# Optimization experiments

Hardware: AMD Instinct MI355X
Metric: run time of the kernel (lower is better)

Reference implementation:

```python
import jax, jax.numpy as jnp
import numpy as np

WIDTH = 256
FREQS = 10
INPUT_WIDTH = 3 + 3 * 2 * FREQS  # 63


def embed_point(point, freqs):
    # point: [N, 3] -> [N, 3*(1+2*freqs)]
    linear = point[..., None]                                  # [N, 3, 1]
    scales = jnp.exp2(jnp.arange(freqs, dtype=point.dtype))    # [freqs]
    angles = linear * scales                                   # [N, 3, freqs]
    emb = jnp.concatenate((linear, jnp.sin(angles), jnp.cos(angles)), axis=-1)
    return emb.reshape(*point.shape[:-1], 3 * (1 + 2 * freqs))


def _xavier(key, fan_in, fan_out):
    limit = jnp.sqrt(6.0 / (fan_in + fan_out)).astype(jnp.float32)
    return jax.random.uniform(key, (fan_in, fan_out), jnp.float32, -limit, limit)


def setup_inputs() -> dict:
    key = jax.random.key(0)
    keys = jax.random.split(key, 20)
    N = 524288
    point = jax.random.normal(keys[0], (N, 3), dtype=jnp.float32)
    dims = [
        (INPUT_WIDTH, WIDTH), (WIDTH, WIDTH), (WIDTH, WIDTH), (WIDTH, WIDTH),
        (WIDTH, WIDTH), (WIDTH + INPUT_WIDTH, WIDTH), (WIDTH, WIDTH),
        (WIDTH, WIDTH), (WIDTH, 4),
    ]
    inp = {"point": point}
    for i, (fi, fo) in enumerate(dims):
        inp[f"w{i}"] = _xavier(keys[1 + i], fi, fo)
        inp[f"b{i}"] = jnp.zeros((fo,), dtype=jnp.float32)
    return inp


def reference(point, w0, b0, w1, b1, w2, b2, w3, b3, w4, b4,
              w5, b5, w6, b6, w7, b7, w8, b8):
    inp = embed_point(point, FREQS)                 # [N, 63]
    x = jax.nn.relu(inp @ w0 + b0)
    x = jax.nn.relu(x @ w1 + b1)
    x = jax.nn.relu(x @ w2 + b2)
    x = jax.nn.relu(x @ w3 + b3)
    x = jax.nn.relu(x @ w4 + b4)
    x = jax.nn.relu(jnp.concatenate((x, inp), -1) @ w5 + b5)  # skip concat
    x = jax.nn.relu(x @ w6 + b6)
    x = jax.nn.relu(x @ w7 + b7)
    return x @ w8 + b8                              # [N, 4]
```

## Files before the change

kernel.cpp:

```cpp
#include <hip/hip_runtime.h>
#include <math.h>


typedef __attribute__((ext_vector_type(8))) short short8;
typedef __attribute__((ext_vector_type(4))) float f32x4;
typedef __attribute__((ext_vector_type(16))) float f32x16;

struct WPtrs { const float* w[8]; };
struct BPtrs { const float* b[8]; };

#define INV2PI 0.15915494309189533577f

#define PK_L0 0
#define PK_L1 16384
#define PK_L2 81920
#define PK_L3 147456
#define PK_L4 212992
#define PK_L5 278528
#define PK_L6 360448
#define PK_L7 425984
#define PK_W8 491520
#define PK_TOTAL 495616

__device__ __forceinline__ unsigned short f2bf(float v) {
  unsigned u = __float_as_uint(v);
  u = u + 0x7fffu + ((u >> 16) & 1u);
  return (unsigned short)(u >> 16);
}
__device__ __forceinline__ float bf_lo(unsigned u) { return __uint_as_float(u << 16); }
__device__ __forceinline__ float bf_hi(unsigned u) { return __uint_as_float(u & 0xffff0000u); }

__device__ __forceinline__ unsigned cvtpk(float a, float b) {
#if __has_builtin(__builtin_amdgcn_cvt_pk_bf16_f32)
  typedef __attribute__((ext_vector_type(2))) __bf16 bf16x2_t;
  bf16x2_t r = __builtin_amdgcn_cvt_pk_bf16_f32(a, b);
  return __builtin_bit_cast(unsigned, r);
#else
  unsigned ua = __float_as_uint(a);
  ua += 0x7fffu + ((ua >> 16) & 1u);
  unsigned ub = __float_as_uint(b);
  ub += 0x7fffu + ((ub >> 16) & 1u);
#if __has_builtin(__builtin_amdgcn_perm)
  return __builtin_amdgcn_perm(ub, ua, 0x07060302u);
#else
  return (ua >> 16) | (ub & 0xffff0000u);
#endif
#endif
}

__device__ __forceinline__ float fractf_(float x) {
#if __has_builtin(__builtin_amdgcn_fract_f32)
  return __builtin_amdgcn_fract_f32(x);
#else
  return x - floorf(x);
#endif
}
__device__ __forceinline__ float sin_rev(float rev) {
#if __has_builtin(__builtin_amdgcn_sinf)
  return __builtin_amdgcn_sinf(rev);
#else
  return __sinf(rev * 6.283185307179586f);
#endif
}

__device__ __forceinline__ float embval(int f, float c0, float c1, float c2,
                                        float x0, float x1, float x2) {
  if (f >= 63) return 0.0f;
  int d = (f >= 21 ? 1 : 0) + (f >= 42 ? 1 : 0);
  int r = f - d * 21;
  float c = (d == 0) ? c0 : (d == 1 ? c1 : c2);
  float x = (d == 0) ? x0 : (d == 1 ? x1 : x2);
  bool isc = r > 10;
  int e = isc ? (r - 11) : (r - 1);
  float rev = fractf_(ldexpf(x, e) + (isc ? 0.25f : 0.0f));
  float s = sin_rev(rev);
  return (r == 0) ? c : s;
}

__device__ __forceinline__ f32x16 mfma32(short8 a, short8 b, f32x16 c) {
  return __builtin_amdgcn_mfma_f32_32x32x16_bf16(a, b, c, 0, 0, 0);
}
__device__ __forceinline__ f32x4 mfma16(short8 a, short8 b, f32x4 c) {
  return __builtin_amdgcn_mfma_f32_16x16x32_bf16(a, b, c, 0, 0, 0);
}

__global__ void pack_weights(WPtrs W, const float* __restrict__ w8,
                             unsigned short* __restrict__ out) {
  int idx = blockIdx.x * 256 + threadIdx.x;
  if (idx >= PK_TOTAL) return;
  float v;
  if (idx >= PK_W8) {
    int t = idx - PK_W8;
    int j = t >> 8, k = t & 255;
    v = (j < 4) ? w8[k * 4 + j] : 0.0f;
  } else {
    int e = idx & 15;
    int blk = idx >> 4;
    int ch = blk & 255;
    int kkg = blk >> 8;
    int l, kk0;
    if      (kkg < 4)   { l = 0; kk0 = 0;   }
    else if (kkg < 20)  { l = 1; kk0 = 4;   }
    else if (kkg < 36)  { l = 2; kk0 = 20;  }
    else if (kkg < 52)  { l = 3; kk0 = 36;  }
    else if (kkg < 68)  { l = 4; kk0 = 52;  }
    else if (kkg < 88)  { l = 5; kk0 = 68;  }
    else if (kkg < 104) { l = 6; kk0 = 88;  }
    else                { l = 7; kk0 = 104; }
    int k = (kkg - kk0) * 16 + e;
    const int realK[8] = {63, 256, 256, 256, 256, 319, 256, 256};
    v = (k < realK[l]) ? W.w[l][k * 256 + ch] : 0.0f;
  }
  out[idx] = f2bf(v);
}

template <int KKA, int PAB, int KKB, bool RB>
__device__ __forceinline__ void do_layer32(
    const unsigned short* srcA, const unsigned short* srcB,
    const unsigned short* __restrict__ wblk,
    const float* __restrict__ bias,
    unsigned short* dst, int w, int n, int h, unsigned swz) {
  f32x16 acc[2][4];
#pragma unroll
  for (int mt = 0; mt < 2; ++mt)
#pragma unroll
    for (int q = 0; q < 4; ++q) {
      f32x4 bq = *reinterpret_cast<const f32x4*>(bias + w * 64 + mt * 32 + q * 8 + h * 4);
#pragma unroll
      for (int nt = 0; nt < 4; ++nt)
#pragma unroll
        for (int r = 0; r < 4; ++r)
          acc[mt][nt][q * 4 + r] = bq[r];
    }

  const char* wb = (const char*)wblk;
  const unsigned aoff = (unsigned)(((w * 64 + n) * 16 + h * 8) * 2);
  const char* rA = (const char*)srcA + (unsigned)(n * PAB);

#define LOAD_A(KK, A0, A1) do {                                      \
    const char* ap_ = wb + (aoff + (unsigned)((KK) * 8192));         \
    A0 = *reinterpret_cast<const short8*>(ap_);                      \
    A1 = *reinterpret_cast<const short8*>(ap_ + 1024);               \
  } while (0)
#define LOAD_B(KK, B0, B1, B2, B3) do {                              \
    unsigned off_ = ((unsigned)((KK) * 32 + h * 16)) ^ swz;          \
    const char* p_ = rA + off_;                                      \
    B0 = *reinterpret_cast<const short8*>(p_);                       \
    B1 = *reinterpret_cast<const short8*>(p_ + 32 * PAB);            \
    B2 = *reinterpret_cast<const short8*>(p_ + 64 * PAB);            \
    B3 = *reinterpret_cast<const short8*>(p_ + 96 * PAB);            \
  } while (0)
#define MFMA8(A0, A1, B0, B1, B2, B3) do {                           \
    acc[0][0] = mfma32(A0, B0, acc[0][0]);                           \
    acc[0][1] = mfma32(A0, B1, acc[0][1]);                           \
    acc[0][2] = mfma32(A0, B2, acc[0][2]);                           \
    acc[0][3] = mfma32(A0, B3, acc[0][3]);                           \
    acc[1][0] = mfma32(A1, B0, acc[1][0]);                           \
    acc[1][1] = mfma32(A1, B1, acc[1][1]);                           \
    acc[1][2] = mfma32(A1, B2, acc[1][2]);                           \
    acc[1][3] = mfma32(A1, B3, acc[1][3]);                           \
  } while (0)

  short8 a0e, a1e, b0e, b1e, b2e, b3e;
  short8 a0o, a1o, b0o, b1o, b2o, b3o;
  LOAD_B(0, b0e, b1e, b2e, b3e);
  LOAD_A(0, a0e, a1e);

#pragma unroll
  for (int kk = 0; kk < KKA; ++kk) {
    if ((kk & 1) == 0) {
      if (kk + 1 < KKA) {
        LOAD_B(kk + 1, b0o, b1o, b2o, b3o);
        LOAD_A(kk + 1, a0o, a1o);
      }
      __builtin_amdgcn_sched_barrier(0);
      __builtin_amdgcn_s_setprio(1);
      MFMA8(a0e, a1e, b0e, b1e, b2e, b3e);
      __builtin_amdgcn_s_setprio(0);
      __builtin_amdgcn_sched_barrier(0);
    } else {
      if (kk + 1 < KKA) {
        LOAD_B(kk + 1, b0e, b1e, b2e, b3e);
        LOAD_A(kk + 1, a0e, a1e);
      }
      __builtin_amdgcn_sched_barrier(0);
      __builtin_amdgcn_s_setprio(1);
      MFMA8(a0o, a1o, b0o, b1o, b2o, b3o);
      __builtin_amdgcn_s_setprio(0);
      __builtin_amdgcn_sched_barrier(0);
    }
  }

  if (KKB > 0) {
    const char* rB = (const char*)srcB + (unsigned)(n * 128);
#pragma unroll
    for (int kl = 0; kl < KKB; ++kl) {
      const char* ab2 = wb + (aoff + (unsigned)((KKA + kl) * 8192));
      short8 a0 = *reinterpret_cast<const short8*>(ab2);
      short8 a1 = *reinterpret_cast<const short8*>(ab2 + 1024);
      unsigned off = ((unsigned)(kl * 32 + h * 16)) ^ swz;
      const char* p = rB + off;
      short8 b0 = *reinterpret_cast<const short8*>(p);
      short8 b1 = *reinterpret_cast<const short8*>(p + 32 * 128);
      short8 b2 = *reinterpret_cast<const short8*>(p + 64 * 128);
      short8 b3 = *reinterpret_cast<const short8*>(p + 96 * 128);
      __builtin_amdgcn_s_setprio(1);
      MFMA8(a0, a1, b0, b1, b2, b3);
      __builtin_amdgcn_s_setprio(0);
    }
  }
#undef LOAD_A
#undef LOAD_B
#undef MFMA8

  if (RB) __syncthreads();
  char* d0 = (char*)dst + (unsigned)(n * 512);
#pragma unroll
  for (int mt = 0; mt < 2; ++mt)
#pragma unroll
    for (int q = 0; q < 4; ++q) {
      unsigned soff = ((unsigned)(w * 128 + mt * 64 + q * 16 + h * 8)) ^ swz;
      char* sp = d0 + soff;
#pragma unroll
      for (int nt = 0; nt < 4; ++nt) {
        float x0 = fmaxf(acc[mt][nt][q * 4 + 0], 0.0f);
        float x1 = fmaxf(acc[mt][nt][q * 4 + 1], 0.0f);
        float x2 = fmaxf(acc[mt][nt][q * 4 + 2], 0.0f);
        float x3 = fmaxf(acc[mt][nt][q * 4 + 3], 0.0f);
        uint2 pr;
        pr.x = cvtpk(x0, x1);
        pr.y = cvtpk(x2, x3);
        *reinterpret_cast<uint2*>(sp + nt * 16384) = pr;
      }
    }
  __syncthreads();
}

__launch_bounds__(256, 2)
__global__ void mlp_mfma(const float* __restrict__ pts, long N,
                         BPtrs B, const float* __restrict__ b8,
                         const unsigned short* __restrict__ wpk,
                         float* __restrict__ out) {
  extern __shared__ unsigned short smem[];
  unsigned short* act = smem;
  unsigned short* emb = smem + 32768;
  const int tid = threadIdx.x;
  const int w = tid >> 6, lane = tid & 63;
  const int n = lane & 31, h = lane >> 5;
  const unsigned swz = (unsigned)((n & 7) << 4);
  const long pbase = (long)blockIdx.x * 128;

  {
    const int pt = tid >> 1, fg = tid & 1;
    const long pg = pbase + pt;
    float c0 = 0.f, c1 = 0.f, c2 = 0.f;
    if (pg < N) {
      const float* pp = pts + pg * 3;
      c0 = __builtin_nontemporal_load(pp);
      c1 = __builtin_nontemporal_load(pp + 1);
      c2 = __builtin_nontemporal_load(pp + 2);
    }
    float x0 = c0 * INV2PI, x1 = c1 * INV2PI, x2 = c2 * INV2PI;
    const unsigned sw = (unsigned)((pt & 7) << 4);
    char* rowp = (char*)emb + (unsigned)(pt * 128);
#pragma unroll
    for (int jb = 0; jb < 2; ++jb) {
      unsigned pk[8];
#pragma unroll
      for (int i = 0; i < 16; i += 2) {
        int f0 = fg * 32 + jb * 16 + i;
        float v0 = embval(f0,     c0, c1, c2, x0, x1, x2);
        float v1 = embval(f0 + 1, c0, c1, c2, x0, x1, x2);
        pk[i >> 1] = cvtpk(v0, v1);
      }
      unsigned base = (unsigned)(fg * 64 + jb * 32);
      *reinterpret_cast<uint4*>(rowp + (base ^ sw)) =
          uint4{pk[0], pk[1], pk[2], pk[3]};
      *reinterpret_cast<uint4*>(rowp + ((base + 16) ^ sw)) =
          uint4{pk[4], pk[5], pk[6], pk[7]};
    }
  }
  __syncthreads();

  do_layer32<4,  128, 0, false>(emb, nullptr, wpk + PK_L0, B.b[0], act, w, n, h, swz);
  do_layer32<16, 512, 0, true >(act, nullptr, wpk + PK_L1, B.b[1], act, w, n, h, swz);
  do_layer32<16, 512, 0, true >(act, nullptr, wpk + PK_L2, B.b[2], act, w, n, h, swz);
  do_layer32<16, 512, 0, true >(act, nullptr, wpk + PK_L3, B.b[3], act, w, n, h, swz);
  do_layer32<16, 512, 0, true >(act, nullptr, wpk + PK_L4, B.b[4], act, w, n, h, swz);
  do_layer32<16, 512, 4, true >(act, emb,     wpk + PK_L5, B.b[5], act, w, n, h, swz);
  do_layer32<16, 512, 0, true >(act, nullptr, wpk + PK_L6, B.b[6], act, w, n, h, swz);
  do_layer32<16, 512, 0, true >(act, nullptr, wpk + PK_L7, B.b[7], act, w, n, h, swz);

  {
    const int l16 = lane & 15, quad = lane >> 4;
    const unsigned short* w8b = wpk + PK_W8 + (unsigned)(l16 * 256 + quad * 8);
    short8 wf[8];
#pragma unroll
    for (int kk = 0; kk < 8; ++kk)
      wf[kk] = *reinterpret_cast<const short8*>(w8b + kk * 32);
    f32x4 bb = *reinterpret_cast<const f32x4*>(b8);
#pragma unroll
    for (int it = 0; it < 2; ++it) {
      const int pt = w * 32 + it * 16 + l16;
      const char* ba = (const char*)act + (unsigned)(pt * 512);
      f32x4 a4 = {0.f, 0.f, 0.f, 0.f};
#pragma unroll
      for (int kk = 0; kk < 8; ++kk) {
        unsigned off = ((unsigned)(kk * 64 + quad * 16)) ^ swz;
        short8 b = *reinterpret_cast<const short8*>(ba + off);
        a4 = mfma16(wf[kk], b, a4);
      }
      if (quad == 0) {
        long pg = pbase + pt;
        f32x4 v = a4 + bb;
        if (pg < N)
          __builtin_nontemporal_store(v, reinterpret_cast<f32x4*>(out + pg * 4));
      }
    }
  }
}

__device__ __forceinline__ unsigned pk2s(float a, float b) {
  return (unsigned)f2bf(a) | ((unsigned)f2bf(b) << 16);
}
__device__ __forceinline__ void fb_seg(const unsigned short* src, int kRows,
                                       const float* __restrict__ wr,
                                       int lane, int ps, float acc[4][16]) {
#pragma unroll 4
  for (int k = 0; k < kRows; ++k) {
    const float* p = wr + k * 256 + lane;
    float w0 = p[0], w1 = p[64], w2 = p[128], w3 = p[192];
    const uint4* xr = reinterpret_cast<const uint4*>(src + ((k << 6) + ps));
    uint4 q0 = xr[0], q1 = xr[1];
    float x[16];
    x[0] = bf_lo(q0.x);  x[1] = bf_hi(q0.x);  x[2] = bf_lo(q0.y);  x[3] = bf_hi(q0.y);
    x[4] = bf_lo(q0.z);  x[5] = bf_hi(q0.z);  x[6] = bf_lo(q0.w);  x[7] = bf_hi(q0.w);
    x[8] = bf_lo(q1.x);  x[9] = bf_hi(q1.x);  x[10] = bf_lo(q1.y); x[11] = bf_hi(q1.y);
    x[12] = bf_lo(q1.z); x[13] = bf_hi(q1.z); x[14] = bf_lo(q1.w); x[15] = bf_hi(q1.w);
#pragma unroll
    for (int pp = 0; pp < 16; ++pp) {
      acc[0][pp] = fmaf(w0, x[pp], acc[0][pp]);
      acc[1][pp] = fmaf(w1, x[pp], acc[1][pp]);
      acc[2][pp] = fmaf(w2, x[pp], acc[2][pp]);
      acc[3][pp] = fmaf(w3, x[pp], acc[3][pp]);
    }
  }
}
__device__ __forceinline__ void fb_layer(const unsigned short* srcA, int kA,
                                         const unsigned short* srcB, int kB,
                                         const float* wrA, const float* wrB,
                                         const float* bias,
                                         unsigned short* dst, int lane, int ps) {
  float acc[4][16];
#pragma unroll
  for (int jt = 0; jt < 4; ++jt) {
    float bb = bias[lane + (jt << 6)];
#pragma unroll
    for (int pp = 0; pp < 16; ++pp) acc[jt][pp] = bb;
  }
  fb_seg(srcA, kA, wrA, lane, ps, acc);
  if (srcB) fb_seg(srcB, kB, wrB, lane, ps, acc);
#pragma unroll
  for (int jt = 0; jt < 4; ++jt) {
    unsigned short* dr = dst + (((lane + (jt << 6)) << 6) + ps);
    float r[16];
#pragma unroll
    for (int pp = 0; pp < 16; ++pp) r[pp] = fmaxf(acc[jt][pp], 0.0f);
    uint4 a, b;
    a.x = pk2s(r[0], r[1]);   a.y = pk2s(r[2], r[3]);
    a.z = pk2s(r[4], r[5]);   a.w = pk2s(r[6], r[7]);
    b.x = pk2s(r[8], r[9]);   b.y = pk2s(r[10], r[11]);
    b.z = pk2s(r[12], r[13]); b.w = pk2s(r[14], r[15]);
    reinterpret_cast<uint4*>(dr)[0] = a;
    reinterpret_cast<uint4*>(dr)[1] = b;
  }
}
__launch_bounds__(256, 2)
__global__ void mlp_fallback(const float* __restrict__ pts, int N,
                             WPtrs W, BPtrs B,
                             const float* __restrict__ w8,
                             const float* __restrict__ b8,
                             float* __restrict__ out) {
  __shared__ unsigned short act[256 * 64];
  __shared__ unsigned short emb[64 * 64];
  const int lane = threadIdx.x & 63;
  const int ps = (threadIdx.x >> 6) << 4;
  const long pbase = (long)blockIdx.x * 64 + ps;
#pragma unroll
  for (int i = 0; i < 16; ++i) {
    int idx = (i << 6) + lane;
    int f = idx >> 4, pp = idx & 15;
    float v = 0.0f;
    if (f < 63) {
      float c = (pbase + pp < N) ? pts[(pbase + pp) * 3 + (f / 21)] : 0.0f;
      float x = c * INV2PI;
      v = embval(f, c, c, c, x, x, x);
    }
    emb[(f << 6) + ps + pp] = f2bf(v);
  }
  fb_layer(emb, 63, nullptr, 0, W.w[0], nullptr, B.b[0], act, lane, ps);
#pragma unroll 1
  for (int l = 1; l <= 4; ++l)
    fb_layer(act, 256, nullptr, 0, W.w[l], nullptr, B.b[l], act, lane, ps);
  fb_layer(act, 256, emb, 63, W.w[5], W.w[5] + 256 * 256, B.b[5], act, lane, ps);
#pragma unroll 1
  for (int l = 6; l <= 7; ++l)
    fb_layer(act, 256, nullptr, 0, W.w[l], nullptr, B.b[l], act, lane, ps);
  {
    const int pp = lane & 15, cc = lane >> 4;
    float a = b8[cc];
#pragma unroll 4
    for (int k = 0; k < 256; ++k)
      a = fmaf(bf_lo((unsigned)act[(k << 6) + ps + pp]), w8[(k << 2) + cc], a);
    if (pbase + pp < N) out[(pbase + pp) * 4 + cc] = a;
  }
}

extern "C" void kernel_launch(void* const* d_in, const int* in_sizes, int n_in,
                              void* d_out, int out_size, void* d_ws, size_t ws_size,
                              hipStream_t stream) {
  const float* pts = (const float*)d_in[0];
  WPtrs W; BPtrs B;
  for (int i = 0; i < 8; ++i) {
    W.w[i] = (const float*)d_in[1 + 2 * i];
    B.b[i] = (const float*)d_in[2 + 2 * i];
  }
  const float* w8 = (const float*)d_in[17];
  const float* b8 = (const float*)d_in[18];
  float* out = (float*)d_out;
  const long N = in_sizes[0] / 3;

  const size_t need = (size_t)PK_TOTAL * sizeof(unsigned short);
  if (ws_size >= need) {
    static hipError_t attr_err = hipFuncSetAttribute(
        reinterpret_cast<const void*>(mlp_mfma),
        hipFuncAttributeMaxDynamicSharedMemorySize, 81920);
    if (attr_err == hipSuccess) {
      unsigned short* wpk = (unsigned short*)d_ws;
      pack_weights<<<1936, 256, 0, stream>>>(W, w8, wpk);
      mlp_mfma<<<(int)((N + 127) / 128), 256, 81920, stream>>>(pts, N, B, b8, wpk, out);
      return;
    }
  }
  mlp_fallback<<<(int)((N + 63) / 64), 256, 0, stream>>>(pts, (int)N, W, B, w8, b8, out);
}
```

Baseline: 533.2 us.

## Deepen LDS operand prefetch to triple-buffered B and paired A loads

New measurement: 537.7 us. About the same (+0.8%).

```diff
diff --git a/kernel.cpp b/kernel.cpp
--- a/kernel.cpp
+++ b/kernel.cpp
@@ -160,35 +160,50 @@
     acc[1][2] = mfma32(A1, B2, acc[1][2]);                           \
     acc[1][3] = mfma32(A1, B3, acc[1][3]);                           \
   } while (0)
-
-  short8 a0e, a1e, b0e, b1e, b2e, b3e;
-  short8 a0o, a1o, b0o, b1o, b2o, b3o;
-  LOAD_B(0, b0e, b1e, b2e, b3e);
-  LOAD_A(0, a0e, a1e);
-
-#pragma unroll
-  for (int kk = 0; kk < KKA; ++kk) {
-    if ((kk & 1) == 0) {
-      if (kk + 1 < KKA) {
-        LOAD_B(kk + 1, b0o, b1o, b2o, b3o);
-        LOAD_A(kk + 1, a0o, a1o);
-      }
-      __builtin_amdgcn_sched_barrier(0);
-      __builtin_amdgcn_s_setprio(1);
-      MFMA8(a0e, a1e, b0e, b1e, b2e, b3e);
-      __builtin_amdgcn_s_setprio(0);
-      __builtin_amdgcn_sched_barrier(0);
-    } else {
-      if (kk + 1 < KKA) {
-        LOAD_B(kk + 1, b0e, b1e, b2e, b3e);
-        LOAD_A(kk + 1, a0e, a1e);
-      }
-      __builtin_amdgcn_sched_barrier(0);
-      __builtin_amdgcn_s_setprio(1);
-      MFMA8(a0o, a1o, b0o, b1o, b2o, b3o);
-      __builtin_amdgcn_s_setprio(0);
-      __builtin_amdgcn_sched_barrier(0);
-    }
+#define LOAD_B_SLOT(KK, S) do {                                      \
+    if ((S) == 0)      LOAD_B(KK, b0_0, b0_1, b0_2, b0_3);           \
+    else if ((S) == 1) LOAD_B(KK, b1_0, b1_1, b1_2, b1_3);           \
+    else               LOAD_B(KK, b2_0, b2_1, b2_2, b2_3);           \
+  } while (0)
+#define MFMA8_SLOT(A0, A1, S) do {                                   \
+    if ((S) == 0)      MFMA8(A0, A1, b0_0, b0_1, b0_2, b0_3);        \
+    else if ((S) == 1) MFMA8(A0, A1, b1_0, b1_1, b1_2, b1_3);        \
+    else               MFMA8(A0, A1, b2_0, b2_1, b2_2, b2_3);        \
+  } while (0)
+
+  static_assert(KKA % 2 == 0, "KKA must be even");
+  short8 b0_0, b0_1, b0_2, b0_3;
+  short8 b1_0, b1_1, b1_2, b1_3;
+  short8 b2_0, b2_1, b2_2, b2_3;
+  short8 aE0a, aE0b, aE1a, aE1b;
+  short8 aO0a, aO0b, aO1a, aO1b;
+
+  LOAD_B(0, b0_0, b0_1, b0_2, b0_3);
+  LOAD_B(1, b1_0, b1_1, b1_2, b1_3);
+  LOAD_A(0, aE0a, aE0b);
+  LOAD_A(1, aE1a, aE1b);
+
+#pragma unroll
+  for (int k = 0; k < KKA / 2; ++k) {
+    const int s0 = (2 * k) % 3, s1 = (2 * k + 1) % 3;
+    const int s2 = (2 * k + 2) % 3, s3 = (2 * k + 3) % 3;
+    const bool even = (k & 1) == 0;
+    if (2 * k + 2 < KKA) {
+      if (even) LOAD_A(2 * k + 2, aO0a, aO0b);
+      else      LOAD_A(2 * k + 2, aE0a, aE0b);
+      LOAD_B_SLOT(2 * k + 2, s2);
+      if (even) LOAD_A(2 * k + 3, aO1a, aO1b);
+      else      LOAD_A(2 * k + 3, aE1a, aE1b);
+    }
+    __builtin_amdgcn_sched_barrier(0);
+    __builtin_amdgcn_s_setprio(1);
+    if (even) MFMA8_SLOT(aE0a, aE0b, s0);
+    else      MFMA8_SLOT(aO0a, aO0b, s0);
+    if (2 * k + 3 < KKA) LOAD_B_SLOT(2 * k + 3, s3);
+    if (even) MFMA8_SLOT(aE1a, aE1b, s1);
+    else      MFMA8_SLOT(aO1a, aO1b, s1);
+    __builtin_amdgcn_s_setprio(0);
+    __builtin_amdgcn_sched_barrier(0);
   }
 
   if (KKB > 0) {
@@ -212,6 +227,8 @@
 #undef LOAD_A
 #undef LOAD_B
 #undef MFMA8
+#undef LOAD_B_SLOT
+#undef MFMA8_SLOT
 
   if (RB) __syncthreads();
   char* d0 = (char*)dst + (unsigned)(n * 512);
```
